# Optimization experiments

Hardware: AMD Instinct MI355X
Metric: run time of the kernel (lower is better)

Reference implementation:

```python
import jax, jax.numpy as jnp
import numpy as np

H, W = 200, 200          # detector resolution
DELX, DELY = 2.0, 2.0    # detector pixel size
EPS = 1e-8


def _rotation(theta, phi, gamma):
    # R = Rz(theta) @ Ry(phi) @ Rx(gamma), as in diffdrr's Rxyz
    ct, st = jnp.cos(theta), jnp.sin(theta)
    cp, sp = jnp.cos(phi), jnp.sin(phi)
    cg, sg = jnp.cos(gamma), jnp.sin(gamma)
    one, zero = jnp.ones_like(ct), jnp.zeros_like(ct)
    Rz = jnp.stack([jnp.stack([ct, -st, zero]), jnp.stack([st, ct, zero]), jnp.stack([zero, zero, one])])
    Ry = jnp.stack([jnp.stack([cp, zero, sp]), jnp.stack([zero, one, zero]), jnp.stack([-sp, zero, cp])])
    Rx = jnp.stack([jnp.stack([one, zero, zero]), jnp.stack([zero, cg, -sg]), jnp.stack([zero, sg, cg])])
    return Rz @ Ry @ Rx


def setup_inputs() -> dict:
    key = jax.random.key(0)
    volume = jax.random.uniform(key, (256, 256, 256), dtype=jnp.float32)
    spacing = jnp.ones((3,), dtype=jnp.float32)
    return {
        "volume": volume,
        "spacing": spacing,
        "sdr": jnp.float32(300.0),
        "theta": jnp.float32(np.pi),
        "phi": jnp.float32(0.0),
        "gamma": jnp.float32(np.pi / 2),
        "bx": jnp.float32(128.0),
        "by": jnp.float32(128.0),
        "bz": jnp.float32(128.0),
    }


def _drr_forward(volume, spacing, sdr, theta, phi, gamma, bx, by, bz):
    # DRR.__init__ flips the volume along axis 0
    vol = volume[::-1]
    nxyz = np.array(vol.shape)  # static shapes: (X, Y, Z)

    # ---- Detector.make_xrays: camera basis, source and detector plane ----
    R = sdr * _rotation(theta, phi, gamma)          # (3,3)
    source = R[:, 0]                                # rho * first column
    center = -source
    u, v = R[:, 1] / sdr, R[:, 2] / sdr             # unit in-plane basis
    t = (jnp.arange(-(H // 2), H // 2) + 1).astype(jnp.float32) * DELX
    s = (jnp.arange(-(W // 2), W // 2) + 1).astype(jnp.float32) * DELY
    trans = jnp.stack([bx, by, bz])
    src = source + trans                            # (3,)
    # cartesian_prod(t, s): row-major (t slow, s fast) -> (H*W, 3)
    tgt = (t[:, None, None] * u + s[None, :, None] * v + center + trans).reshape(H * W, 3)

    # ---- Siddon.raytrace ----
    sdd = tgt - src + EPS                           # (n, 3)
    # alpha values at every axis-aligned voxel boundary plane
    ax = (jnp.arange(nxyz[0] + 1, dtype=jnp.float32) * spacing[0] - src[0]) / sdd[:, 0:1]
    ay = (jnp.arange(nxyz[1] + 1, dtype=jnp.float32) * spacing[1] - src[1]) / sdd[:, 1:2]
    az = (jnp.arange(nxyz[2] + 1, dtype=jnp.float32) * spacing[2] - src[2]) / sdd[:, 2:3]
    alphas = jnp.concatenate([ax, ay, az], axis=-1)  # (n, P) with P = X+Y+Z+3

    # entry/exit alphas of the volume bounding box
    a0 = (0.0 - src) / sdd                           # (n, 3)
    a1 = (nxyz.astype(np.float32) * spacing - src) / sdd
    amin = jnp.max(jnp.minimum(a0, a1), axis=-1, keepdims=True)
    amax = jnp.min(jnp.maximum(a0, a1), axis=-1, keepdims=True)

    good = (alphas >= amin) & (alphas <= amax)
    alphas = jnp.sort(jnp.where(good, alphas, jnp.inf), axis=-1)  # invalid -> +inf at end

    amid = 0.5 * (alphas[:, :-1] + alphas[:, 1:])    # (n, P-1)
    step = alphas[:, 1:] - alphas[:, :-1]            # inf-inf -> nan for padding
    valid = jnp.isfinite(step)

    # midpoint positions -> voxel indices (trunc, as in torch .trunc())
    pts = src + amid[..., None] * sdd[:, None, :]    # (n, P-1, 3)
    idx = jnp.trunc(jnp.where(valid[..., None], pts, 0.0) / spacing).astype(jnp.int32)
    idx = jnp.clip(idx, 0, jnp.asarray(nxyz - 1, dtype=jnp.int32))
    vox = vol[idx[..., 0], idx[..., 1], idx[..., 2]]  # (n, P-1) gather

    drr = jnp.sum(jnp.where(valid, step, 0.0) * vox, axis=-1)  # nansum equivalent
    drr = drr * jnp.linalg.norm(tgt - src + EPS, axis=-1)       # scale by ray length
    return drr.reshape(1, 1, H, W)


def reference(volume, spacing, sdr, theta, phi, gamma, bx, by, bz):
    return _drr_forward(volume, spacing, sdr, theta, phi, gamma, bx, by, bz)
```

## Files before the change

### kernel.cpp

```cpp
#include <hip/hip_runtime.h>
#include <math.h>

#pragma clang fp contract(off)

#define SPLIT 16
static constexpr int HH = 200, WW = 200;
static constexpr int NRAY = HH * WW;

__device__ __forceinline__ float alpha_of(float k, float sp, float src, float sdd) {
    return (k * sp - src) / sdd;
}

template<bool UNIT>
__device__ __forceinline__ float merge_loop(
    const float* __restrict__ vol, float bhi, float prev,
    float kf0, float kf1, float kf2,
    float kst0, float kst1, float kst2,
    float na0, float na1, float na2,
    float src0, float src1, float src2,
    float spn0, float spn1, float spn2,
    float sdd0, float sdd1, float sdd2)
{
    float acc = 0.0f;
    for (int g = 0; g < 1024; ++g) {
        const float q = fminf(fminf(na0, na1), na2);
        if (!(q <= bhi)) break;

        const float step = q - prev;
        const float amid = 0.5f * (prev + q);

        const float p0 = src0 + amid * sdd0;
        const float p1 = src1 + amid * sdd1;
        const float p2 = src2 + amid * sdd2;
        float f0, f1, f2;
        if (UNIT) { f0 = p0; f1 = p1; f2 = p2; }
        else      { f0 = p0 / spn0; f1 = p1 / spn1; f2 = p2 / spn2; }
        f0 = fminf(fmaxf(f0, 0.0f), 255.0f);
        f1 = fminf(fmaxf(f1, 0.0f), 255.0f);
        f2 = fminf(fmaxf(f2, 0.0f), 255.0f);
        const int i0 = (int)f0, i1 = (int)f1, i2 = (int)f2;

        const int addr = ((((255 ^ i0) << 8) + i1) << 8) + i2;
        acc = fmaf(step, vol[addr], acc);
        prev = q;

        const bool m0 = (na0 == q);
        const bool m1 = !m0 && (na1 == q);
        const float kf_s  = m0 ? kf0  : (m1 ? kf1  : kf2);
        const float kst_s = m0 ? kst0 : (m1 ? kst1 : kst2);
        const float sr_s  = m0 ? src0 : (m1 ? src1 : src2);
        const float sd_s  = m0 ? sdd0 : (m1 ? sdd1 : sdd2);
        const float nk = kf_s + kst_s;
        float al;
        if (UNIT) {
            al = (nk - sr_s) / sd_s;
        } else {
            const float sp_s = m0 ? spn0 : (m1 ? spn1 : spn2);
            al = (nk * sp_s - sr_s) / sd_s;
        }
        const float nv = (nk >= 0.0f && nk <= 256.0f) ? al : INFINITY;
        if (m0)      { kf0 = nk; na0 = nv; }
        else if (m1) { kf1 = nk; na1 = nv; }
        else         { kf2 = nk; na2 = nv; }
    }
    return acc;
}

__global__ __launch_bounds__(256)
void drr_kernel(const float* __restrict__ vol,
                const float* __restrict__ spacing,
                const float* __restrict__ sdrP,
                const float* __restrict__ thetaP,
                const float* __restrict__ phiP,
                const float* __restrict__ gammaP,
                const float* __restrict__ bxP,
                const float* __restrict__ byP,
                const float* __restrict__ bzP,
                float* __restrict__ out)
{
    const int tid = blockIdx.x * blockDim.x + threadIdx.x;
    if (tid >= NRAY * SPLIT) return;
    const int seg = tid / NRAY;
    const int rid = tid - seg * NRAY;
    const int it  = rid % HH;
    const int is  = rid / HH;

    const float sdr = sdrP[0];
    const float th = thetaP[0], ph = phiP[0], ga = gammaP[0];
    const float ct = cosf(th), st = sinf(th);
    const float cp = cosf(ph), sp = sinf(ph);
    const float cg = cosf(ga), sg = sinf(ga);

    const float rot[3][3] = {
        { ct*cp, ct*sp*sg - st*cg, ct*sp*cg + st*sg },
        { st*cp, st*sp*sg + ct*cg, st*sp*cg - ct*sg },
        { -sp,   cp*sg,            cp*cg            }
    };

    float u[3], v[3], source[3], trans[3], src[3], spn[3];
    trans[0] = bxP[0]; trans[1] = byP[0]; trans[2] = bzP[0];
    for (int a = 0; a < 3; ++a) {
        source[a] = sdr * rot[a][0];
        u[a] = (sdr * rot[a][1]) / sdr;
        v[a] = (sdr * rot[a][2]) / sdr;
        src[a] = source[a] + trans[a];
        spn[a] = spacing[a];
    }

    const float tc = (float)(it - HH/2 + 1) * 2.0f;
    const float sc = (float)(is - WW/2 + 1) * 2.0f;

    float sdd[3];
    float nrm2 = 0.0f;
    for (int a = 0; a < 3; ++a) {
        float tg = tc * u[a] + sc * v[a];
        tg = tg - source[a];
        tg = tg + trans[a];
        float dd = (tg - src[a]) + 1e-8f;
        sdd[a] = dd;
        nrm2 = nrm2 + dd * dd;
    }
    const bool unit = (spn[0] == 1.0f) & (spn[1] == 1.0f) & (spn[2] == 1.0f);

    float amin = -INFINITY, amax = INFINITY;
    for (int a = 0; a < 3; ++a) {
        float a0 = (0.0f - src[a]) / sdd[a];
        float a1 = (256.0f * spn[a] - src[a]) / sdd[a];
        amin = fmaxf(amin, fminf(a0, a1));
        amax = fminf(amax, fmaxf(a0, a1));
    }

    float acc = 0.0f;
    if (amax > amin) {
        const float blo = (seg == 0) ? amin
                        : amin + (amax - amin) * ((float)seg / (float)SPLIT);
        const float bhi = (seg == SPLIT - 1) ? amax
                        : amin + (amax - amin) * ((float)(seg + 1) / (float)SPLIT);

        float kf[3], kst[3], nexta[3];
        float prev = -INFINITY;

        for (int a = 0; a < 3; ++a) {
            const float sd = sdd[a], sr = src[a], spv = spn[a];
            const bool pos = sd > 0.0f;
            kst[a] = pos ? 1.0f : -1.0f;
            const float kseed = (blo * sd + sr) / spv;
            int kk;
            if (pos) {
                kk = (int)floorf(kseed) + 1;
                kk = kk < 0 ? 0 : (kk > 257 ? 257 : kk);
                while (kk > 0    && alpha_of((float)(kk-1), spv, sr, sd) >  blo) --kk;
                while (kk <= 256 && alpha_of((float)kk,     spv, sr, sd) <= blo) ++kk;
                if (kk - 1 >= 0) {
                    float ap = alpha_of((float)(kk-1), spv, sr, sd);
                    if (ap >= amin && ap > prev) prev = ap;
                }
                nexta[a] = (kk <= 256) ? alpha_of((float)kk, spv, sr, sd) : INFINITY;
            } else {
                kk = (int)ceilf(kseed) - 1;
                kk = kk > 256 ? 256 : (kk < -1 ? -1 : kk);
                while (kk < 256 && alpha_of((float)(kk+1), spv, sr, sd) >  blo) ++kk;
                while (kk >= 0  && alpha_of((float)kk,     spv, sr, sd) <= blo) --kk;
                if (kk + 1 <= 256) {
                    float ap = alpha_of((float)(kk+1), spv, sr, sd);
                    if (ap >= amin && ap > prev) prev = ap;
                }
                nexta[a] = (kk >= 0) ? alpha_of((float)kk, spv, sr, sd) : INFINITY;
            }
            kf[a] = (float)kk;
        }

        if (unit) {
            acc = merge_loop<true >(vol, bhi, prev,
                                    kf[0], kf[1], kf[2], kst[0], kst[1], kst[2],
                                    nexta[0], nexta[1], nexta[2],
                                    src[0], src[1], src[2],
                                    spn[0], spn[1], spn[2],
                                    sdd[0], sdd[1], sdd[2]);
        } else {
            acc = merge_loop<false>(vol, bhi, prev,
                                    kf[0], kf[1], kf[2], kst[0], kst[1], kst[2],
                                    nexta[0], nexta[1], nexta[2],
                                    src[0], src[1], src[2],
                                    spn[0], spn[1], spn[2],
                                    sdd[0], sdd[1], sdd[2]);
        }
    }

    atomicAdd(&out[it * WW + is], acc * sqrtf(nrm2));
}

extern "C" void kernel_launch(void* const* d_in, const int* in_sizes, int n_in,
                              void* d_out, int out_size, void* d_ws, size_t ws_size,
                              hipStream_t stream)
{
    const float* vol     = (const float*)d_in[0];
    const float* spacing = (const float*)d_in[1];
    const float* sdr     = (const float*)d_in[2];
    const float* theta   = (const float*)d_in[3];
    const float* phi     = (const float*)d_in[4];
    const float* gamma   = (const float*)d_in[5];
    const float* bx      = (const float*)d_in[6];
    const float* by      = (const float*)d_in[7];
    const float* bz      = (const float*)d_in[8];
    float* out = (float*)d_out;

    hipMemsetAsync(out, 0, (size_t)out_size * sizeof(float), stream);

    const int threads = NRAY * SPLIT;
    const int block   = 256;
    const int grid    = threads / block;
    drr_kernel<<<grid, block, 0, stream>>>(vol, spacing, sdr, theta, phi, gamma,
                                           bx, by, bz, out);
}
```

Measured before the change: 59.25 us.

## Precompute trip count and use incremental alpha stepping in Siddon merge loop

Each segment now seeds both its start and end plane indices, so the number of intervals is known up front and the merge loop runs a fixed trip count with no per-step bound comparison. Next-plane alpha values are advanced by adding a constant delta instead of a divide each step. The loop is unrolled by two so the two voxel gathers can be in flight together. SPLIT changes from 16 to 13 and the grid is rounded up. Accumulating alpha by repeated addition can drift from the exact per-plane divides and change the plane ordering, which risks small numerical differences.

```diff
diff --git a/kernel.cpp b/kernel.cpp
--- a/kernel.cpp
+++ b/kernel.cpp
@@ -3,7 +3,7 @@
 
 #pragma clang fp contract(off)
 
-#define SPLIT 16
+#define SPLIT 13
 static constexpr int HH = 200, WW = 200;
 static constexpr int NRAY = HH * WW;
 
@@ -11,57 +11,70 @@
     return (k * sp - src) / sdd;
 }
 
+__device__ __forceinline__ int seed_ptr(float X, float spv, float sr, float sd, bool pos) {
+    const float kf = (X * sd + sr) / spv;
+    int kk;
+    if (pos) {
+        kk = (int)floorf(kf) + 1;
+        kk = kk < 0 ? 0 : (kk > 257 ? 257 : kk);
+        while (kk > 0    && alpha_of((float)(kk-1), spv, sr, sd) >  X) --kk;
+        while (kk <= 256 && alpha_of((float)kk,     spv, sr, sd) <= X) ++kk;
+    } else {
+        kk = (int)ceilf(kf) - 1;
+        kk = kk > 256 ? 256 : (kk < -1 ? -1 : kk);
+        while (kk < 256 && alpha_of((float)(kk+1), spv, sr, sd) >  X) ++kk;
+        while (kk >= 0  && alpha_of((float)kk,     spv, sr, sd) <= X) --kk;
+    }
+    return kk;
+}
+
+#define INTERVAL(qv, stepv, voxv)                                        \
+    const float qv = fminf(fminf(tM0, tM1), tM2);                        \
+    const float stepv = qv - prev;                                       \
+    {   const float amid = 0.5f * (prev + qv);                           \
+        const float p0 = src0 + amid * sdd0;                             \
+        const float p1 = src1 + amid * sdd1;                             \
+        const float p2 = src2 + amid * sdd2;                             \
+        float f0, f1, f2;                                                \
+        if (UNIT) { f0 = p0; f1 = p1; f2 = p2; }                         \
+        else      { f0 = p0 / spn0; f1 = p1 / spn1; f2 = p2 / spn2; }    \
+        f0 = fminf(fmaxf(f0, 0.0f), 255.0f);                             \
+        f1 = fminf(fmaxf(f1, 0.0f), 255.0f);                             \
+        f2 = fminf(fmaxf(f2, 0.0f), 255.0f);                             \
+        const int i0 = (int)f0, i1 = (int)f1, i2 = (int)f2;              \
+        const int addr = ((((255 ^ i0) << 8) + i1) << 8) + i2;           \
+        voxv = vol[addr]; }                                              \
+    prev = qv;                                                           \
+    {   const bool m0 = (tM0 == qv);                                     \
+        const bool m1 = !m0 && (tM1 == qv);                              \
+        const bool m2 = !(m0 || m1);                                     \
+        tM0 = m0 ? tM0 + dl0 : tM0;                                      \
+        tM1 = m1 ? tM1 + dl1 : tM1;                                      \
+        tM2 = m2 ? tM2 + dl2 : tM2; }
+
 template<bool UNIT>
 __device__ __forceinline__ float merge_loop(
-    const float* __restrict__ vol, float bhi, float prev,
-    float kf0, float kf1, float kf2,
-    float kst0, float kst1, float kst2,
-    float na0, float na1, float na2,
+    const float* __restrict__ vol, int trip, float prev,
+    float tM0, float tM1, float tM2,
+    float dl0, float dl1, float dl2,
     float src0, float src1, float src2,
     float spn0, float spn1, float spn2,
     float sdd0, float sdd1, float sdd2)
 {
     float acc = 0.0f;
-    for (int g = 0; g < 1024; ++g) {
-        const float q = fminf(fminf(na0, na1), na2);
-        if (!(q <= bhi)) break;
-
-        const float step = q - prev;
-        const float amid = 0.5f * (prev + q);
-
-        const float p0 = src0 + amid * sdd0;
-        const float p1 = src1 + amid * sdd1;
-        const float p2 = src2 + amid * sdd2;
-        float f0, f1, f2;
-        if (UNIT) { f0 = p0; f1 = p1; f2 = p2; }
-        else      { f0 = p0 / spn0; f1 = p1 / spn1; f2 = p2 / spn2; }
-        f0 = fminf(fmaxf(f0, 0.0f), 255.0f);
-        f1 = fminf(fmaxf(f1, 0.0f), 255.0f);
-        f2 = fminf(fmaxf(f2, 0.0f), 255.0f);
-        const int i0 = (int)f0, i1 = (int)f1, i2 = (int)f2;
-
-        const int addr = ((((255 ^ i0) << 8) + i1) << 8) + i2;
-        acc = fmaf(step, vol[addr], acc);
-        prev = q;
-
-        const bool m0 = (na0 == q);
-        const bool m1 = !m0 && (na1 == q);
-        const float kf_s  = m0 ? kf0  : (m1 ? kf1  : kf2);
-        const float kst_s = m0 ? kst0 : (m1 ? kst1 : kst2);
-        const float sr_s  = m0 ? src0 : (m1 ? src1 : src2);
-        const float sd_s  = m0 ? sdd0 : (m1 ? sdd1 : sdd2);
-        const float nk = kf_s + kst_s;
-        float al;
-        if (UNIT) {
-            al = (nk - sr_s) / sd_s;
-        } else {
-            const float sp_s = m0 ? spn0 : (m1 ? spn1 : spn2);
-            al = (nk * sp_s - sr_s) / sd_s;
-        }
-        const float nv = (nk >= 0.0f && nk <= 256.0f) ? al : INFINITY;
-        if (m0)      { kf0 = nk; na0 = nv; }
-        else if (m1) { kf1 = nk; na1 = nv; }
-        else         { kf2 = nk; na2 = nv; }
+    int n = trip;
+    while (n >= 2) {
+        float voxA, voxB;
+        INTERVAL(qA, stepA, voxA)
+        INTERVAL(qB, stepB, voxB)
+        acc = fmaf(stepA, voxA, acc);
+        acc = fmaf(stepB, voxB, acc);
+        n -= 2;
+    }
+    if (n > 0) {
+        float voxC;
+        INTERVAL(qC, stepC, voxC)
+        acc = fmaf(stepC, voxC, acc);
     }
     return acc;
 }
@@ -137,50 +150,45 @@
         const float bhi = (seg == SPLIT - 1) ? amax
                         : amin + (amax - amin) * ((float)(seg + 1) / (float)SPLIT);
 
-        float kf[3], kst[3], nexta[3];
+        float tM[3], dl[3];
         float prev = -INFINITY;
+        int trip = 0;
 
         for (int a = 0; a < 3; ++a) {
             const float sd = sdd[a], sr = src[a], spv = spn[a];
             const bool pos = sd > 0.0f;
-            kst[a] = pos ? 1.0f : -1.0f;
-            const float kseed = (blo * sd + sr) / spv;
-            int kk;
+            const int ks = seed_ptr(blo, spv, sr, sd, pos);
+            const int ke = seed_ptr(bhi, spv, sr, sd, pos);
+            int cnt;
             if (pos) {
-                kk = (int)floorf(kseed) + 1;
-                kk = kk < 0 ? 0 : (kk > 257 ? 257 : kk);
-                while (kk > 0    && alpha_of((float)(kk-1), spv, sr, sd) >  blo) --kk;
-                while (kk <= 256 && alpha_of((float)kk,     spv, sr, sd) <= blo) ++kk;
-                if (kk - 1 >= 0) {
-                    float ap = alpha_of((float)(kk-1), spv, sr, sd);
+                cnt = ke - ks;
+                if (ks - 1 >= 0) {
+                    const float ap = alpha_of((float)(ks-1), spv, sr, sd);
                     if (ap >= amin && ap > prev) prev = ap;
                 }
-                nexta[a] = (kk <= 256) ? alpha_of((float)kk, spv, sr, sd) : INFINITY;
+                tM[a] = (ks <= 256) ? alpha_of((float)ks, spv, sr, sd) : INFINITY;
             } else {
-                kk = (int)ceilf(kseed) - 1;
-                kk = kk > 256 ? 256 : (kk < -1 ? -1 : kk);
-                while (kk < 256 && alpha_of((float)(kk+1), spv, sr, sd) >  blo) ++kk;
-                while (kk >= 0  && alpha_of((float)kk,     spv, sr, sd) <= blo) --kk;
-                if (kk + 1 <= 256) {
-                    float ap = alpha_of((float)(kk+1), spv, sr, sd);
+                cnt = ks - ke;
+                if (ks + 1 <= 256) {
+                    const float ap = alpha_of((float)(ks+1), spv, sr, sd);
                     if (ap >= amin && ap > prev) prev = ap;
                 }
-                nexta[a] = (kk >= 0) ? alpha_of((float)kk, spv, sr, sd) : INFINITY;
+                tM[a] = (ks >= 0) ? alpha_of((float)ks, spv, sr, sd) : INFINITY;
             }
-            kf[a] = (float)kk;
+            if (cnt < 0) cnt = 0;
+            trip += cnt;
+            dl[a] = fabsf(spv / sd);
         }
 
         if (unit) {
-            acc = merge_loop<true >(vol, bhi, prev,
-                                    kf[0], kf[1], kf[2], kst[0], kst[1], kst[2],
-                                    nexta[0], nexta[1], nexta[2],
+            acc = merge_loop<true >(vol, trip, prev,
+                                    tM[0], tM[1], tM[2], dl[0], dl[1], dl[2],
                                     src[0], src[1], src[2],
                                     spn[0], spn[1], spn[2],
                                     sdd[0], sdd[1], sdd[2]);
         } else {
-            acc = merge_loop<false>(vol, bhi, prev,
-                                    kf[0], kf[1], kf[2], kst[0], kst[1], kst[2],
-                                    nexta[0], nexta[1], nexta[2],
+            acc = merge_loop<false>(vol, trip, prev,
+                                    tM[0], tM[1], tM[2], dl[0], dl[1], dl[2],
                                     src[0], src[1], src[2],
                                     spn[0], spn[1], spn[2],
                                     sdd[0], sdd[1], sdd[2]);
@@ -209,7 +217,7 @@
 
     const int threads = NRAY * SPLIT;
     const int block   = 256;
-    const int grid    = threads / block;
+    const int grid    = (threads + block - 1) / block;
     drr_kernel<<<grid, block, 0, stream>>>(vol, spacing, sdr, theta, phi, gamma,
                                            bx, by, bz, out);
 }
```

Result: faster. 57.24 us (-3.4%).
